# Kernel tuning notes

Hardware: AMD Instinct MI355X
Metric: run time of the kernel (lower is better)

The kernel has to match this reference:

```python
import jax, jax.numpy as jnp
import numpy as np

B, N, C, K1, K2, TD = 4, 4096, 128, 16, 8, 64
CIN = 2 * (3 + C)  # 262


def setup_inputs() -> dict:
    key = jax.random.key(0)
    ks = jax.random.split(key, 8)
    s = 0.05
    feature = jax.random.normal(ks[0], (B, C, N), jnp.float32)
    xyz = jax.random.normal(ks[1], (B, 3, N), jnp.float32)
    wq = jax.random.normal(ks[2], (TD, CIN), jnp.float32) * s
    wk = jax.random.normal(ks[3], (TD, CIN), jnp.float32) * s
    wv = jax.random.normal(ks[4], (TD, CIN), jnp.float32) * s
    w1 = jax.random.normal(ks[5], (C, TD), jnp.float32) * s
    bq = jnp.zeros((TD,), jnp.float32)
    bk = jnp.zeros((TD,), jnp.float32)
    bv = jnp.zeros((TD,), jnp.float32)
    b1 = jnp.zeros((C,), jnp.float32)
    return {"feature": feature, "xyz": xyz, "wq": wq, "bq": bq,
            "wk": wk, "bk": bk, "wv": wv, "bv": bv, "w1": w1, "b1": b1}


def _group(x, ind):
    # x: [B, Cx, N], ind: [B, N, K] -> [B, Cx, K, N]; g[b,c,k,n] = x[b,c,ind[b,n,k]]
    g = jnp.take_along_axis(x[:, :, None, :], ind[:, None, :, :], axis=3)  # [B,Cx,N,K]
    return g.transpose(0, 1, 3, 2)


def reference(feature, xyz, wq, bq, wk, bk, wv, bv, w1, b1):
    # --- KNN (self-included then dropped), idx[b,n,k] = k-th nearest of point n ---
    sq = jnp.sum(xyz * xyz, axis=1)                                   # [B,N]
    dist = sq[:, :, None] + sq[:, None, :] - 2.0 * jnp.einsum('bdn,bdm->bnm', xyz, xyz)
    _, idx = jax.lax.top_k(-dist, K1 + 1)                             # [B,N,17]
    idx = idx[:, :, 1:]                                               # drop self -> [B,N,16]
    idx1 = idx[:, :, :K2]                                             # [B,N,8]

    gxyz = _group(xyz, idx)        # [B,3,16,N]
    gxyz1 = _group(xyz, idx1)      # [B,3,8,N]
    gfea = _group(feature, idx)    # [B,C,16,N]
    gfea1 = _group(feature, idx1)  # [B,C,8,N]

    rel_xyz = gxyz - xyz[:, :, None, :]
    rel_xyz1 = gxyz1 - xyz[:, :, None, :]
    rel_fea = gfea - feature[:, :, None, :]
    rel_fea1 = gfea1 - feature[:, :, None, :]

    def relpos(rx, rf, K):
        return jnp.concatenate([
            rx,
            jnp.broadcast_to(xyz[:, :, None, :], (B, 3, K, N)),
            rf,
            jnp.broadcast_to(feature[:, :, None, :], (B, C, K, N)),
        ], axis=1)  # [B,262,K,N]

    rel_pos = relpos(rel_xyz, rel_fea, K1)     # [B,262,16,N]
    rel_pos1 = relpos(rel_xyz1, rel_fea1, K2)  # [B,262,8,N]

    # 1x1 Conv2d projections
    q = jnp.einsum('oc,bckn->bokn', wq, rel_pos1) + bq[None, :, None, None]  # [B,64,8,N]
    k = jnp.einsum('oc,bckn->bokn', wk, rel_pos) + bk[None, :, None, None]   # [B,64,16,N]
    v = jnp.einsum('oc,bckn->bokn', wv, rel_pos) + bv[None, :, None, None]   # [B,64,16,N]

    attn = jnp.einsum('bmnf,bmjf->bnjf', q, k)   # [B,8,16,N]
    attn = jax.nn.softmax(attn, axis=-2)         # softmax over j (16 neighbors)
    res = jnp.einsum('bnjf,bmjf->bmf', attn, v)  # [B,64,N]

    out = jnp.einsum('om,bmf->bof', w1, res) + b1[None, :, None]  # Conv1d 64->128
    return out + feature
```

## Files before the change

### kernel.cpp

```cpp
#include <hip/hip_runtime.h>

#define NN 4096
#define CCH 128

__global__ __launch_bounds__(256) void transpose_w(
    const float* __restrict__ wq, const float* __restrict__ wk, const float* __restrict__ wv,
    const float* __restrict__ w1, const float* __restrict__ xyz,
    float* __restrict__ wTq, float* __restrict__ wTk, float* __restrict__ wTv,
    float* __restrict__ w1T, float* __restrict__ wPack, float4* __restrict__ pts4) {
  int t = blockIdx.x * 256 + threadIdx.x;
  if (t < 64 * 262) {
    int o = t / 262, c = t - o * 262;
    wTq[c * 64 + o] = wq[t];
    wTk[c * 64 + o] = wk[t];
    wTv[c * 64 + o] = wv[t];
  }
  if (t < 128 * 64) {
    int r = t >> 6, c2 = t & 63;
    w1T[c2 * 128 + r] = w1[t];
  }
  if (t < 49152) {
    int r = t & 3, o = (t >> 2) & 63;
    int g = t >> 8;
    int ct = g / 6, mh = g - ct * 6;
    int m = mh >> 1, h = mh & 1;
    const float* wsrc = (m == 0) ? wq : ((m == 1) ? wk : wv);
    wPack[t] = wsrc[o * 262 + (h ? 134 : 6) + 4 * ct + r];
  }
  if (t < 4 * NN) {
    int bb = t >> 12, i = t & 4095;
    const float* xb = xyz + (size_t)bb * 3 * NN;
    float x = xb[i], y = xb[NN + i], z = xb[2 * NN + i];
    pts4[t] = make_float4(x, y, z, x * x + y * y + z * z);
  }
}

__global__ __launch_bounds__(1024, 4) void knn_half(const float4* __restrict__ pts4,
                                                    unsigned long long* __restrict__ keys_ws) {
  __shared__ float bufA[64 * 64];
  __shared__ float bufB[64 * 64];
  __shared__ unsigned long long hits[32 * 65];
  __shared__ int cnt[64];
  const int b  = blockIdx.x >> 7;
  const int g  = (blockIdx.x >> 1) & 63;
  const int h  = blockIdx.x & 1;
  const int n0 = g << 6;
  const int ql = threadIdx.x & 63;
  const int ch = __builtin_amdgcn_readfirstlane(threadIdx.x >> 6);
  if (threadIdx.x < 64) cnt[threadIdx.x] = 0;
  const int q = n0 + ql;
  const float4* pb4 = pts4 + ((size_t)b << 12);
  const float4 me = pb4[q];
  float bd0 = 3.0e38f, bd1 = 3.0e38f, bd2 = 3.0e38f, bd3 = 3.0e38f;
  const int m0 = (h << 11) + (ch << 7);
  for (int mb = m0; mb < m0 + 128; mb += 8) {
    float4 P[8];
#pragma unroll
    for (int u = 0; u < 8; ++u) P[u] = pb4[mb + u];
#pragma unroll
    for (int u = 0; u < 8; ++u) {
      float d = me.w + P[u].w - 2.0f * (me.x * P[u].x + me.y * P[u].y + me.z * P[u].z);
      d = (mb + u == q) ? 3.0e38f : d;
      bd3 = __builtin_amdgcn_fmed3f(d, bd2, bd3);
      bd2 = __builtin_amdgcn_fmed3f(d, bd1, bd2);
      bd1 = __builtin_amdgcn_fmed3f(d, bd0, bd1);
      bd0 = fminf(bd0, d);
    }
  }
  {
    const int r0 = (ch * 4) * 64 + ql;
    bufA[r0] = bd0; bufA[r0 + 64] = bd1; bufA[r0 + 128] = bd2; bufA[r0 + 192] = bd3;
  }
  __syncthreads();
  if (ch < 8) {
    const int a0 = (2 * ch) * 4, b0 = (2 * ch + 1) * 4;
    float o8[8]; int pa = 0, pb = 0;
#pragma unroll
    for (int k = 0; k < 8; ++k) {
      float va = (pa < 4) ? bufA[(a0 + pa) * 64 + ql] : 3.0e38f;
      float vb = (pb < 4) ? bufA[(b0 + pb) * 64 + ql] : 3.0e38f;
      bool ta = va <= vb;
      o8[k] = ta ? va : vb;
      pa += ta ? 1 : 0; pb += ta ? 0 : 1;
    }
#pragma unroll
    for (int k = 0; k < 8; ++k) bufB[(ch * 8 + k) * 64 + ql] = o8[k];
  }
  __syncthreads();
  if (ch < 4) {
    const int a0 = (2 * ch) * 8, b0 = (2 * ch + 1) * 8;
    float o16[16]; int pa = 0, pb = 0;
#pragma unroll
    for (int k = 0; k < 16; ++k) {
      float va = (pa < 8) ? bufB[(a0 + pa) * 64 + ql] : 3.0e38f;
      float vb = (pb < 8) ? bufB[(b0 + pb) * 64 + ql] : 3.0e38f;
      bool ta = va <= vb;
      o16[k] = ta ? va : vb;
      pa += ta ? 1 : 0; pb += ta ? 0 : 1;
    }
#pragma unroll
    for (int k = 0; k < 16; ++k) bufA[(ch * 16 + k) * 64 + ql] = o16[k];
  }
  __syncthreads();
  if (ch < 2) {
    const int a0 = (2 * ch) * 16, b0 = (2 * ch + 1) * 16;
    float o16[16]; int pa = 0, pb = 0;
#pragma unroll
    for (int k = 0; k < 16; ++k) {
      float va = bufA[(a0 + pa) * 64 + ql];
      float vb = bufA[(b0 + pb) * 64 + ql];
      bool ta = va <= vb;
      o16[k] = ta ? va : vb;
      pa += ta ? 1 : 0; pb += ta ? 0 : 1;
    }
#pragma unroll
    for (int k = 0; k < 16; ++k) bufB[(ch * 16 + k) * 64 + ql] = o16[k];
  }
  __syncthreads();
  if (ch == 0) {
    float v = 0.f; int pa = 0, pb = 0;
#pragma unroll
    for (int k = 0; k < 16; ++k) {
      float va = bufB[pa * 64 + ql];
      float vb = bufB[(16 + pb) * 64 + ql];
      bool ta = va <= vb;
      v = ta ? va : vb;
      pa += ta ? 1 : 0; pb += ta ? 0 : 1;
    }
    bufA[15 * 64 + ql] = v;
  }
  __syncthreads();
  const float tau = bufA[15 * 64 + ql];
  for (int mb = m0; mb < m0 + 128; mb += 8) {
    float4 P[8];
#pragma unroll
    for (int u = 0; u < 8; ++u) P[u] = pb4[mb + u];
#pragma unroll
    for (int u = 0; u < 8; ++u) {
      float d = me.w + P[u].w - 2.0f * (me.x * P[u].x + me.y * P[u].y + me.z * P[u].z);
      if (d <= tau && (mb + u) != q) {
        int pos = atomicAdd(&cnt[ql], 1);
        if (pos < 32) {
          unsigned int f = __float_as_uint(d);
          f ^= (f >> 31) ? 0xFFFFFFFFu : 0x80000000u;
          hits[pos * 65 + ql] = ((unsigned long long)f << 32) | (unsigned int)(mb + u);
        }
      }
    }
  }
  __syncthreads();
  const int l5 = threadIdx.x & 31;
#pragma unroll
  for (int t = 0; t < 2; ++t) {
    const int qq = (t * 1024 + (int)threadIdx.x) >> 5;
    int nv = cnt[qq]; nv = nv > 32 ? 32 : nv;
    unsigned long long key = (l5 < nv) ? hits[l5 * 65 + qq] : ~0ULL;
#pragma unroll
    for (int k = 2; k <= 32; k <<= 1) {
#pragma unroll
      for (int jm = k >> 1; jm > 0; jm >>= 1) {
        unsigned long long o2 = __shfl_xor(key, jm, 32);
        bool asc = ((l5 & k) == 0);
        bool lower = ((l5 & jm) == 0);
        unsigned long long mn = key < o2 ? key : o2;
        unsigned long long mx = key < o2 ? o2 : key;
        key = (lower == asc) ? mn : mx;
      }
    }
    if (l5 < 16) {
      const size_t gq = (size_t)((b << 12) + n0 + qq);
      keys_ws[((size_t)h << 18) + gq * 16 + l5] = key;
    }
  }
}

__global__ __launch_bounds__(256) void knn_merge(const unsigned long long* __restrict__ keys_ws,
                                                 int* __restrict__ idxout) {
  const int gq = blockIdx.x * 256 + threadIdx.x;
  const unsigned long long* A  = keys_ws + (size_t)gq * 16;
  const unsigned long long* Bp = keys_ws + (1u << 18) + (size_t)gq * 16;
  int* op = idxout + (size_t)gq * 16;
  int pa = 0, pb = 0;
#pragma unroll
  for (int k = 0; k < 16; ++k) {
    unsigned long long va = A[pa], vb = Bp[pb];
    bool ta = va <= vb;
    op[k] = (int)((ta ? va : vb) & 0xFFFFFFFFu);
    pa += ta ? 1 : 0; pb += ta ? 0 : 1;
  }
}

__global__ __launch_bounds__(512) void proj_kernel(
    const float* __restrict__ feature, const float* __restrict__ xyz,
    const float* __restrict__ wTq, const float* __restrict__ wTk, const float* __restrict__ wTv,
    const float* __restrict__ wPack,
    const float* __restrict__ bq, const float* __restrict__ bk, const float* __restrict__ bv,
    float* __restrict__ uq, float* __restrict__ cq,
    float* __restrict__ uk, float* __restrict__ ck,
    float* __restrict__ uv, float* __restrict__ cv) {
  __shared__ float fl[64][132];
  __shared__ float4 wl[2 * 32 * 64];
  const int p0 = blockIdx.x << 6;
  const int b  = p0 >> 12;
  const int n0 = p0 & 4095;
  {
    const int i  = threadIdx.x & 63;
    const int c0 = threadIdx.x >> 6;
    const float* fb = feature + (size_t)b * CCH * NN + n0 + i;
    for (int cc = c0; cc < CCH; cc += 8) fl[i][cc] = fb[(size_t)cc * NN];
    if (threadIdx.x < 192) {
      const int d = threadIdx.x >> 6;
      fl[i][128 + d] = xyz[((size_t)b * 3 + d) * NN + n0 + i];
    }
  }
  const int o  = threadIdx.x & 63;
  const int pg = threadIdx.x >> 6;
  const float4* wp = reinterpret_cast<const float4*>(wPack);

  for (int m = 0; m < 3; ++m) {
    __syncthreads();
    for (int d4 = threadIdx.x; d4 < 4096; d4 += 512) {
      const int h = d4 >> 11, ct = (d4 >> 6) & 31, oo = d4 & 63;
      wl[d4] = wp[(ct * 6 + m * 2 + h) * 64 + oo];
    }
    __syncthreads();
    float aU[8], aT[8];
#pragma unroll
    for (int s = 0; s < 8; ++s) { aU[s] = 0.f; aT[s] = 0.f; }
    for (int ct = 0; ct < 32; ++ct) {
      const float4 wu = wl[ct * 64 + o];
      const float4 wt = wl[2048 + ct * 64 + o];
#pragma unroll
      for (int s = 0; s < 8; ++s) {
        const float4 f4 = *reinterpret_cast<const float4*>(&fl[pg * 8 + s][4 * ct]);
        aU[s] += wu.x * f4.x + wu.y * f4.y + wu.z * f4.z + wu.w * f4.w;
        aT[s] += wt.x * f4.x + wt.y * f4.y + wt.z * f4.z + wt.w * f4.w;
      }
    }
    const float* wtm = (m == 0) ? wTq : ((m == 1) ? wTk : wTv);
    float wxu[3], wxt[3];
#pragma unroll
    for (int dd = 0; dd < 3; ++dd) { wxu[dd] = wtm[dd * 64 + o]; wxt[dd] = wtm[(3 + dd) * 64 + o]; }
    const float bo = ((m == 0) ? bq : ((m == 1) ? bk : bv))[o];
    float* um = (m == 0) ? uq : ((m == 1) ? uk : uv);
    float* cm = (m == 0) ? cq : ((m == 1) ? ck : cv);
#pragma unroll
    for (int s = 0; s < 8; ++s) {
      const int p = pg * 8 + s;
      const float x = fl[p][128], y = fl[p][129], z = fl[p][130];
      const size_t gp = ((size_t)(p0 + p)) * 64 + o;
      const float uu = aU[s] + wxu[0] * x + wxu[1] * y + wxu[2] * z;
      const float tt = aT[s] + wxt[0] * x + wxt[1] * y + wxt[2] * z;
      um[gp] = uu; cm[gp] = tt + bo - uu;
    }
  }
}

__global__ __launch_bounds__(256) void attn_core(
    const int* __restrict__ idx,
    const float* __restrict__ uq, const float* __restrict__ cq,
    const float* __restrict__ uk, const float* __restrict__ ck,
    const float* __restrict__ uv, const float* __restrict__ cv,
    float* __restrict__ res_ws) {
  __shared__ float kq[4][24][68];
  const int slot = threadIdx.x >> 6;
  const int o    = threadIdx.x & 63;
  const int p = (blockIdx.x << 2) + slot;
  const int b = p >> 12;
  const int myidx = idx[(size_t)p * 16 + (o & 15)];
  const size_t pb = (size_t)p * 64 + o;
  const float cqo = cq[pb], cko = ck[pb], cvo = cv[pb];
  const int rowbase = (b << 12) * 64;
  float v[16];
#pragma unroll
  for (int j = 0; j < 16; ++j) {
    int nb = __shfl(myidx, j);
    int row = rowbase + nb * 64 + o;
    kq[slot][j][o] = uk[row] + cko;
    v[j] = uv[row] + cvo;
    if (j < 8) kq[slot][16 + j][o] = uq[row] + cqo;
  }
  const int i  = o >> 3;
  const int jj = o & 7;
  const float* qrow = &kq[slot][16 + i][0];
  const float* k0r  = &kq[slot][jj][0];
  const float* k1r  = &kq[slot][8 + jj][0];
  float s0 = 0.f, s1 = 0.f;
#pragma unroll
  for (int t = 0; t < 16; ++t) {
    float4 q4 = *reinterpret_cast<const float4*>(qrow + 4 * t);
    float4 a4 = *reinterpret_cast<const float4*>(k0r + 4 * t);
    float4 c4 = *reinterpret_cast<const float4*>(k1r + 4 * t);
    s0 += q4.x * a4.x + q4.y * a4.y + q4.z * a4.z + q4.w * a4.w;
    s1 += q4.x * c4.x + q4.y * c4.y + q4.z * c4.z + q4.w * c4.w;
  }
  float mx = fmaxf(s0, s1);
  mx = fmaxf(mx, __shfl_xor(mx, 1));
  mx = fmaxf(mx, __shfl_xor(mx, 2));
  mx = fmaxf(mx, __shfl_xor(mx, 4));
  float e0 = __expf(s0 - mx), e1 = __expf(s1 - mx);
  float den = e0 + e1;
  den += __shfl_xor(den, 1);
  den += __shfl_xor(den, 2);
  den += __shfl_xor(den, 4);
  const float inv = 1.0f / den;
  float w0 = e0 * inv, w1s = e1 * inv;
  w0 += __shfl_xor(w0, 8);   w1s += __shfl_xor(w1s, 8);
  w0 += __shfl_xor(w0, 16);  w1s += __shfl_xor(w1s, 16);
  w0 += __shfl_xor(w0, 32);  w1s += __shfl_xor(w1s, 32);
  float res = 0.f;
#pragma unroll
  for (int j = 0; j < 8; ++j) {
    res += __shfl(w0, j)  * v[j];
    res += __shfl(w1s, j) * v[j + 8];
  }
  res_ws[pb] = res;
}

__global__ __launch_bounds__(512) void out_kernel(
    const float* __restrict__ feature, const float* __restrict__ res,
    const float* __restrict__ w1T, const float* __restrict__ b1,
    float* __restrict__ out) {
  __shared__ float rT[64][66];
  const int p0 = blockIdx.x << 6;
  const int b  = p0 >> 12;
  const int n0 = p0 & 4095;
  {
    const int o = threadIdx.x & 63;
    for (int pp = threadIdx.x >> 6; pp < 64; pp += 8)
      rT[o][pp] = res[(size_t)(p0 + pp) * 64 + o];
  }
  __syncthreads();
  const int n = threadIdx.x & 63;
  const int c0 = (threadIdx.x >> 6) * 16;
  float acc[16];
#pragma unroll
  for (int cc = 0; cc < 16; ++cc) acc[cc] = b1[c0 + cc];
  for (int o = 0; o < 64; ++o) {
    const float rr = rT[o][n];
    const float* wrow = &w1T[o * 128 + c0];
#pragma unroll
    for (int cc = 0; cc < 16; ++cc) acc[cc] += wrow[cc] * rr;
  }
#pragma unroll
  for (int cc = 0; cc < 16; ++cc) {
    const size_t gi = ((size_t)(b * 128 + c0 + cc) << 12) + n0 + n;
    out[gi] = acc[cc] + feature[gi];
  }
}

extern "C" void kernel_launch(void* const* d_in, const int* in_sizes, int n_in,
                              void* d_out, int out_size, void* d_ws, size_t ws_size,
                              hipStream_t stream) {
  const float* feature = (const float*)d_in[0];
  const float* xyz     = (const float*)d_in[1];
  const float* wq      = (const float*)d_in[2];
  const float* bq      = (const float*)d_in[3];
  const float* wk      = (const float*)d_in[4];
  const float* bk      = (const float*)d_in[5];
  const float* wv      = (const float*)d_in[6];
  const float* bv      = (const float*)d_in[7];
  const float* w1      = (const float*)d_in[8];
  const float* b1      = (const float*)d_in[9];
  float* out = (float*)d_out;

  char* ws = (char*)d_ws;
  int*    idx  = (int*)ws;
  float4* pts4 = (float4*)(ws + (1u << 20));
  float* uq  = (float*)(ws + (2u << 20));
  float* cq  = uq + (1u << 20);
  float* uk  = cq + (1u << 20);
  float* ck  = uk + (1u << 20);
  float* uv  = ck + (1u << 20);
  float* cv  = uv + (1u << 20);
  float* res = cv + (1u << 20);
  float* wTq = res + (1u << 20);
  float* wTk = wTq + 262 * 64;
  float* wTv = wTk + 262 * 64;
  float* w1T = wTv + 262 * 64;
  float* wPk = w1T + 128 * 64;
  unsigned long long* keys = (unsigned long long*)(ws + (2u << 20));

  transpose_w<<<192, 256, 0, stream>>>(wq, wk, wv, w1, xyz, wTq, wTk, wTv, w1T, wPk, pts4);
  knn_half<<<512, 1024, 0, stream>>>(pts4, keys);
  knn_merge<<<64, 256, 0, stream>>>(keys, idx);
  proj_kernel<<<256, 512, 0, stream>>>(feature, xyz, wTq, wTk, wTv, wPk, bq, bk, bv,
                                       uq, cq, uk, ck, uv, cv);
  attn_core<<<4096, 256, 0, stream>>>(idx, uq, cq, uk, ck, uv, cv, res);
  out_kernel<<<256, 512, 0, stream>>>(feature, res, w1T, b1, out);
}
```

Baseline: 218.6 us.

## Fuse Q/K/V projection passes and interleave K and V into float2 buffer

The projection kernel now computes all three Q/K/V projections in one sweep over the shared feature tile, loading the packed weights in two halves instead of three separate passes. This triples the accumulator register count per thread. K and V neighbour values are stored interleaved as float2, so the attention gather fetches both with one 8-byte load per neighbour instead of two scattered 4-byte loads. Workspace offsets are re-laid out to fit the new buffers, and the higher register pressure may reduce occupancy.

```diff
diff --git a/kernel.cpp b/kernel.cpp
--- a/kernel.cpp
+++ b/kernel.cpp
@@ -195,11 +195,11 @@
     const float* __restrict__ wTq, const float* __restrict__ wTk, const float* __restrict__ wTv,
     const float* __restrict__ wPack,
     const float* __restrict__ bq, const float* __restrict__ bk, const float* __restrict__ bv,
-    float* __restrict__ uq, float* __restrict__ cq,
-    float* __restrict__ uk, float* __restrict__ ck,
-    float* __restrict__ uv, float* __restrict__ cv) {
+    float* __restrict__ uqA, float* __restrict__ cq,
+    float2* __restrict__ ukv,
+    float* __restrict__ ck, float* __restrict__ cv) {
   __shared__ float fl[64][132];
-  __shared__ float4 wl[2 * 32 * 64];
+  __shared__ float4 wl[16 * 6 * 64];
   const int p0 = blockIdx.x << 6;
   const int b  = p0 >> 12;
   const int n0 = p0 & 4095;
@@ -216,51 +216,66 @@
   const int o  = threadIdx.x & 63;
   const int pg = threadIdx.x >> 6;
   const float4* wp = reinterpret_cast<const float4*>(wPack);
-
-  for (int m = 0; m < 3; ++m) {
+  float aU[3][8], aT[3][8];
+#pragma unroll
+  for (int mm = 0; mm < 3; ++mm)
+#pragma unroll
+    for (int s = 0; s < 8; ++s) { aU[mm][s] = 0.f; aT[mm][s] = 0.f; }
+
+  for (int half = 0; half < 2; ++half) {
     __syncthreads();
-    for (int d4 = threadIdx.x; d4 < 4096; d4 += 512) {
-      const int h = d4 >> 11, ct = (d4 >> 6) & 31, oo = d4 & 63;
-      wl[d4] = wp[(ct * 6 + m * 2 + h) * 64 + oo];
-    }
+    for (int d4 = threadIdx.x; d4 < 6144; d4 += 512)
+      wl[d4] = wp[half * 6144 + d4];
     __syncthreads();
-    float aU[8], aT[8];
-#pragma unroll
-    for (int s = 0; s < 8; ++s) { aU[s] = 0.f; aT[s] = 0.f; }
-    for (int ct = 0; ct < 32; ++ct) {
-      const float4 wu = wl[ct * 64 + o];
-      const float4 wt = wl[2048 + ct * 64 + o];
+#pragma unroll 4
+    for (int ct = 0; ct < 16; ++ct) {
+      float4 w4[6];
+#pragma unroll
+      for (int mh = 0; mh < 6; ++mh) w4[mh] = wl[(ct * 6 + mh) * 64 + o];
+      const int cglob = half * 16 + ct;
 #pragma unroll
       for (int s = 0; s < 8; ++s) {
-        const float4 f4 = *reinterpret_cast<const float4*>(&fl[pg * 8 + s][4 * ct]);
-        aU[s] += wu.x * f4.x + wu.y * f4.y + wu.z * f4.z + wu.w * f4.w;
-        aT[s] += wt.x * f4.x + wt.y * f4.y + wt.z * f4.z + wt.w * f4.w;
+        const float4 f4 = *reinterpret_cast<const float4*>(&fl[pg * 8 + s][4 * cglob]);
+#pragma unroll
+        for (int mm = 0; mm < 3; ++mm) {
+          aU[mm][s] += w4[2 * mm].x * f4.x + w4[2 * mm].y * f4.y + w4[2 * mm].z * f4.z + w4[2 * mm].w * f4.w;
+          aT[mm][s] += w4[2 * mm + 1].x * f4.x + w4[2 * mm + 1].y * f4.y + w4[2 * mm + 1].z * f4.z + w4[2 * mm + 1].w * f4.w;
+        }
       }
     }
-    const float* wtm = (m == 0) ? wTq : ((m == 1) ? wTk : wTv);
-    float wxu[3], wxt[3];
-#pragma unroll
-    for (int dd = 0; dd < 3; ++dd) { wxu[dd] = wtm[dd * 64 + o]; wxt[dd] = wtm[(3 + dd) * 64 + o]; }
-    const float bo = ((m == 0) ? bq : ((m == 1) ? bk : bv))[o];
-    float* um = (m == 0) ? uq : ((m == 1) ? uk : uv);
-    float* cm = (m == 0) ? cq : ((m == 1) ? ck : cv);
-#pragma unroll
-    for (int s = 0; s < 8; ++s) {
-      const int p = pg * 8 + s;
-      const float x = fl[p][128], y = fl[p][129], z = fl[p][130];
-      const size_t gp = ((size_t)(p0 + p)) * 64 + o;
-      const float uu = aU[s] + wxu[0] * x + wxu[1] * y + wxu[2] * z;
-      const float tt = aT[s] + wxt[0] * x + wxt[1] * y + wxt[2] * z;
-      um[gp] = uu; cm[gp] = tt + bo - uu;
-    }
+  }
+  float wxu[3][3], wxt[3][3];
+#pragma unroll
+  for (int dd = 0; dd < 3; ++dd) {
+    wxu[0][dd] = wTq[dd * 64 + o]; wxt[0][dd] = wTq[(3 + dd) * 64 + o];
+    wxu[1][dd] = wTk[dd * 64 + o]; wxt[1][dd] = wTk[(3 + dd) * 64 + o];
+    wxu[2][dd] = wTv[dd * 64 + o]; wxt[2][dd] = wTv[(3 + dd) * 64 + o];
+  }
+  const float bo0 = bq[o], bo1 = bk[o], bo2 = bv[o];
+#pragma unroll
+  for (int s = 0; s < 8; ++s) {
+    const int p = pg * 8 + s;
+    const float x = fl[p][128], y = fl[p][129], z = fl[p][130];
+    const size_t gp = ((size_t)(p0 + p)) * 64 + o;
+    float uu, tt;
+    uu = aU[0][s] + wxu[0][0] * x + wxu[0][1] * y + wxu[0][2] * z;
+    tt = aT[0][s] + wxt[0][0] * x + wxt[0][1] * y + wxt[0][2] * z;
+    uqA[gp] = uu; cq[gp] = tt + bo0 - uu;
+    const float uk_ = aU[1][s] + wxu[1][0] * x + wxu[1][1] * y + wxu[1][2] * z;
+    tt = aT[1][s] + wxt[1][0] * x + wxt[1][1] * y + wxt[1][2] * z;
+    ck[gp] = tt + bo1 - uk_;
+    const float uv_ = aU[2][s] + wxu[2][0] * x + wxu[2][1] * y + wxu[2][2] * z;
+    tt = aT[2][s] + wxt[2][0] * x + wxt[2][1] * y + wxt[2][2] * z;
+    cv[gp] = tt + bo2 - uv_;
+    ukv[gp] = make_float2(uk_, uv_);
   }
 }
 
 __global__ __launch_bounds__(256) void attn_core(
     const int* __restrict__ idx,
-    const float* __restrict__ uq, const float* __restrict__ cq,
-    const float* __restrict__ uk, const float* __restrict__ ck,
-    const float* __restrict__ uv, const float* __restrict__ cv,
+    const float* __restrict__ uqA, const float* __restrict__ cq,
+    const float2* __restrict__ ukv,
+    const float* __restrict__ ck, const float* __restrict__ cv,
     float* __restrict__ res_ws) {
   __shared__ float kq[4][24][68];
   const int slot = threadIdx.x >> 6;
@@ -276,9 +291,10 @@
   for (int j = 0; j < 16; ++j) {
     int nb = __shfl(myidx, j);
     int row = rowbase + nb * 64 + o;
-    kq[slot][j][o] = uk[row] + cko;
-    v[j] = uv[row] + cvo;
-    if (j < 8) kq[slot][16 + j][o] = uq[row] + cqo;
+    float2 kv = ukv[row];
+    kq[slot][j][o] = kv.x + cko;
+    v[j] = kv.y + cvo;
+    if (j < 8) kq[slot][16 + j][o] = uqA[row] + cqo;
   }
   const int i  = o >> 3;
   const int jj = o & 7;
@@ -367,25 +383,24 @@
   char* ws = (char*)d_ws;
   int*    idx  = (int*)ws;
   float4* pts4 = (float4*)(ws + (1u << 20));
-  float* uq  = (float*)(ws + (2u << 20));
-  float* cq  = uq + (1u << 20);
-  float* uk  = cq + (1u << 20);
-  float* ck  = uk + (1u << 20);
-  float* uv  = ck + (1u << 20);
-  float* cv  = uv + (1u << 20);
-  float* res = cv + (1u << 20);
-  float* wTq = res + (1u << 20);
-  float* wTk = wTq + 262 * 64;
-  float* wTv = wTk + 262 * 64;
-  float* w1T = wTv + 262 * 64;
-  float* wPk = w1T + 128 * 64;
+  float*  uqA  = (float*)(ws + (2u << 20));
+  float*  cq   = (float*)(ws + (6u << 20));
+  float*  ck   = (float*)(ws + (10u << 20));
+  float*  cv   = (float*)(ws + (14u << 20));
+  float2* ukv  = (float2*)(ws + (18u << 20));
+  float*  res  = (float*)(ws + (26u << 20));
+  float*  wTq  = (float*)(ws + (30u << 20));
+  float*  wTk  = wTq + 262 * 64;
+  float*  wTv  = wTk + 262 * 64;
+  float*  w1T  = wTv + 262 * 64;
+  float*  wPk  = w1T + 128 * 64;
   unsigned long long* keys = (unsigned long long*)(ws + (2u << 20));
 
   transpose_w<<<192, 256, 0, stream>>>(wq, wk, wv, w1, xyz, wTq, wTk, wTv, w1T, wPk, pts4);
   knn_half<<<512, 1024, 0, stream>>>(pts4, keys);
   knn_merge<<<64, 256, 0, stream>>>(keys, idx);
   proj_kernel<<<256, 512, 0, stream>>>(feature, xyz, wTq, wTk, wTv, wPk, bq, bk, bv,
-                                       uq, cq, uk, ck, uv, cv);
-  attn_core<<<4096, 256, 0, stream>>>(idx, uq, cq, uk, ck, uv, cv, res);
+                                       uqA, cq, ukv, ck, cv);
+  attn_core<<<4096, 256, 0, stream>>>(idx, uqA, cq, ukv, ck, cv, res);
   out_kernel<<<256, 512, 0, stream>>>(feature, res, w1T, b1, out);
 }
```

After: 218.3 us. No clear change (-0.1%).
